# Performance work log

Measured on AMD Instinct MI355X. Metric: run time of the kernel, lower is better.

The kernel has to match this reference:

```python
import jax, jax.numpy as jnp
import numpy as np

B, S, CTX, DIM = 2, 2048, 2048, 2048
H, HKV, HD = 16, 4, 128
HID = 5464  # 4*ceil(int(4*DIM*2/3)/4)
EPS = 1.1920929e-07  # torch eps=None -> finfo(fp32).eps
REP = H // HKV


def rmsnorm(x, w):
    return x * jax.lax.rsqrt(jnp.mean(x * x, axis=-1, keepdims=True) + EPS) * w


def rotate_half(x):
    # interleaved rotate: out[::2] = -x[1::2], out[1::2] = x[::2]
    x2 = x.reshape(x.shape[:-1] + (-1, 2))
    return jnp.stack([-x2[..., 1], x2[..., 0]], axis=-1).reshape(x.shape)


def masked_attn(q, k, v, mask):
    # q,k,v: [B,H,Sq/Sk,D]; mask broadcastable to [B,H,Sq,Sk]
    scale = 1.0 / jnp.sqrt(jnp.asarray(q.shape[-1], q.dtype))
    s = jnp.einsum('bhqd,bhkd->bhqk', q, k) * scale
    s = jnp.where(mask, s, jnp.asarray(-1e30, s.dtype))
    p = jax.nn.softmax(s, axis=-1)
    p = jnp.where(mask, p, 0.0)  # fully-masked rows -> 0 output (flex_attention semantics)
    return jnp.einsum('bhqk,bhkd->bhqd', p, v)


def setup_inputs() -> dict:
    key = jax.random.key(0)
    ks = jax.random.split(key, 20)
    std = 0.02
    return {
        'x': jax.random.normal(ks[0], (B, S, DIM), jnp.float32),
        'context': jax.random.normal(ks[1], (B, CTX, DIM), jnp.float32),
        'freqs_cos': jax.random.uniform(ks[2], (S, 1, HD), jnp.float32),
        'freqs_sin': jax.random.uniform(ks[3], (S, 1, HD), jnp.float32),
        'wqkv': jax.random.normal(ks[4], ((H + 2 * HKV) * HD, DIM), jnp.float32) * std,
        'wo_self': jax.random.normal(ks[5], (DIM, DIM), jnp.float32) * std,
        'qn_self': jnp.ones((HD,), jnp.float32),
        'kn_self': jnp.ones((HD,), jnp.float32),
        'wq': jax.random.normal(ks[6], (H * HD, DIM), jnp.float32) * std,
        'wkv': jax.random.normal(ks[7], (2 * HKV * HD, DIM), jnp.float32) * std,
        'wo_cross': jax.random.normal(ks[8], (DIM, DIM), jnp.float32) * std,
        'qn_cross': jnp.ones((HD,), jnp.float32),
        'kn_cross': jnp.ones((HD,), jnp.float32),
        'w1': jax.random.normal(ks[9], (HID, DIM), jnp.float32) * std,
        'w2': jax.random.normal(ks[10], (DIM, HID), jnp.float32) * std,
        'attn_norm_w': jnp.ones((DIM,), jnp.float32),
        'cross_norm_w': jnp.ones((DIM,), jnp.float32),
        'ffn_norm_w': jnp.ones((DIM,), jnp.float32),
        'vis_mask': jax.random.randint(ks[11], (B, S), 0, 2).astype(bool),
        'context_mask': jax.random.randint(ks[12], (B, CTX), 0, 2).astype(bool),
    }


def reference(x, context, freqs_cos, freqs_sin, wqkv, wo_self, qn_self, kn_self,
              wq, wkv, wo_cross, qn_cross, kn_cross, w1, w2,
              attn_norm_w, cross_norm_w, ffn_norm_w, vis_mask, context_mask):
    b, s, _ = x.shape
    ctx = context.shape[1]

    # ---- self-attention (prenorm) ----
    h0 = rmsnorm(x, attn_norm_w)
    qkv = h0 @ wqkv.T
    xq = qkv[..., :H * HD].reshape(b, s, H, HD)
    xk = qkv[..., H * HD:(H + HKV) * HD].reshape(b, s, HKV, HD)
    xv = qkv[..., (H + HKV) * HD:].reshape(b, s, HKV, HD)
    xq = rmsnorm(xq, qn_self)   # qk-norm BEFORE rope in self-attn
    xk = rmsnorm(xk, kn_self)
    xq = xq * freqs_cos + rotate_half(xq) * freqs_sin
    xk = xk * freqs_cos + rotate_half(xk) * freqs_sin
    q = xq.transpose(0, 2, 1, 3)
    k = jnp.repeat(xk.transpose(0, 2, 1, 3), REP, axis=1)
    v = jnp.repeat(xv.transpose(0, 2, 1, 3), REP, axis=1)
    m_self = vis_mask[:, None, :, None] & vis_mask[:, None, None, :]
    a = masked_attn(q, k, v, m_self)
    h = x + a.transpose(0, 2, 1, 3).reshape(b, s, DIM) @ wo_self.T

    # ---- cross-attention (prenorm) ----
    hc = rmsnorm(h, cross_norm_w)
    xq = (hc @ wq.T).reshape(b, s, H, HD)
    kv = context @ wkv.T
    xk = kv[..., :HKV * HD].reshape(b, ctx, HKV, HD)
    xv = kv[..., HKV * HD:].reshape(b, ctx, HKV, HD)
    xq = xq * freqs_cos + rotate_half(xq) * freqs_sin  # rope on q BEFORE qk-norm in cross-attn
    xq = rmsnorm(xq, qn_cross)
    xk = rmsnorm(xk, kn_cross)
    q = xq.transpose(0, 2, 1, 3)
    k = jnp.repeat(xk.transpose(0, 2, 1, 3), REP, axis=1)
    v = jnp.repeat(xv.transpose(0, 2, 1, 3), REP, axis=1)
    m_cross = context_mask[:, None, None, :]
    a = masked_attn(q, k, v, m_cross)
    h = h + a.transpose(0, 2, 1, 3).reshape(b, s, DIM) @ wo_cross.T

    # ---- FFN (silu) ----
    hf = rmsnorm(h, ffn_norm_w)
    return h + jax.nn.silu(hf @ w1.T) @ w2.T
```

## Files before the change

### kernel.cpp

```cpp
#include <hip/hip_runtime.h>

#define DEVI __device__ __forceinline__

typedef __attribute__((ext_vector_type(4))) float f32x4;
typedef __attribute__((ext_vector_type(8))) __bf16 bf16x8;

static constexpr float EPS = 1.1920929e-07f;
static constexpr float SC2L = 0.12751551960234575f;

DEVI float bf2f(unsigned short u){ return __uint_as_float(((unsigned)u)<<16); }
DEVI unsigned short f2bfu(float f){
  unsigned u = __float_as_uint(f);
  u += 0x7fffu + ((u>>16)&1u);
  return (unsigned short)(u>>16);
}
DEVI unsigned pack2(float a, float b){ return (unsigned)f2bfu(a) | ((unsigned)f2bfu(b)<<16); }
DEVI float exp2a(float x){ float r; asm("v_exp_f32 %0, %1" : "=v"(r) : "v"(x)); return r; }
DEVI unsigned cvtpk(float lo, float hi){
  unsigned r; asm("v_cvt_pk_bf16_f32 %0, %1, %2" : "=v"(r) : "v"(lo), "v"(hi)); return r;
}

DEVI void gload16(const void* g, const void* l){
  __builtin_amdgcn_global_load_lds((const __attribute__((address_space(1))) void*)g,
                                   (__attribute__((address_space(3))) void*)l, 16, 0, 0);
}

__global__ void k_masknorm(const unsigned* __restrict__ vin, const unsigned* __restrict__ cin,
                           unsigned char* __restrict__ vout, unsigned char* __restrict__ cout){
  __shared__ int smode;
  const int t = threadIdx.x;
  if (t==0) smode = 0;
  __syncthreads();
  unsigned loc = 0;
  for (int i=t; i<1024; i+=256) loc |= (vin[i] > 1u);
  if (loc) smode = 1;
  __syncthreads();
  if (smode){
    for (int i=t; i<1024; i+=256){
      ((unsigned*)vout)[i] = vin[i];
      ((unsigned*)cout)[i] = cin[i];
    }
  } else {
    const int* vi = (const int*)vin; const int* ci = (const int*)cin;
    for (int i=t; i<4096; i+=256){
      vout[i] = (unsigned char)(vi[i] != 0);
      cout[i] = (unsigned char)(ci[i] != 0);
    }
  }
}

__global__ void k_conv(const float* __restrict__ s, unsigned short* __restrict__ d, int n4){
  int i = blockIdx.x*256 + threadIdx.x;
  if (i >= n4) return;
  float4 v = ((const float4*)s)[i];
  uint2 u; u.x = pack2(v.x, v.y); u.y = pack2(v.z, v.w);
  ((uint2*)d)[i] = u;
}
__global__ void k_convpad_rows(const float* __restrict__ s, unsigned short* __restrict__ d,
                               int R, int C, int Rp){
  int i = blockIdx.x*256 + threadIdx.x;
  int total = (Rp*C)>>2;
  if (i >= total) return;
  uint2 u; u.x = 0u; u.y = 0u;
  if (i*4 < R*C){ float4 v = ((const float4*)s)[i]; u.x = pack2(v.x,v.y); u.y = pack2(v.z,v.w); }
  ((uint2*)d)[i] = u;
}
__global__ void k_convpad_cols(const float* __restrict__ s, unsigned short* __restrict__ d,
                               int N, int K, int Kp){
  int i = blockIdx.x*256 + threadIdx.x;
  int total = (N*Kp)>>2;
  if (i >= total) return;
  int i4 = i*4; int n = i4/Kp; int k = i4 - n*Kp;
  uint2 u; u.x = 0u; u.y = 0u;
  if (k < K){ float4 v = *(const float4*)(s + (size_t)n*K + k); u.x = pack2(v.x,v.y); u.y = pack2(v.z,v.w); }
  ((uint2*)d)[i] = u;
}

__global__ void k_rms(const float* __restrict__ X, const float* __restrict__ W,
                      unsigned short* __restrict__ Y){
  const int row = blockIdx.x, tid = threadIdx.x;
  const float* x = X + (size_t)row*2048;
  float4 v0 = ((const float4*)x)[tid*2];
  float4 v1 = ((const float4*)x)[tid*2+1];
  float ss = v0.x*v0.x+v0.y*v0.y+v0.z*v0.z+v0.w*v0.w
           + v1.x*v1.x+v1.y*v1.y+v1.z*v1.z+v1.w*v1.w;
  #pragma unroll
  for (int o=32;o;o>>=1) ss += __shfl_xor(ss, o);
  __shared__ float red[4];
  if ((tid&63)==0) red[tid>>6] = ss;
  __syncthreads();
  float tot = red[0]+red[1]+red[2]+red[3];
  float rs = rsqrtf(tot*(1.0f/2048.0f) + EPS);
  float4 w0 = ((const float4*)W)[tid*2];
  float4 w1 = ((const float4*)W)[tid*2+1];
  uint4 u;
  u.x = pack2(v0.x*rs*w0.x, v0.y*rs*w0.y);
  u.y = pack2(v0.z*rs*w0.z, v0.w*rs*w0.w);
  u.z = pack2(v1.x*rs*w1.x, v1.y*rs*w1.y);
  u.w = pack2(v1.z*rs*w1.z, v1.w*rs*w1.w);
  *(uint4*)(Y + (size_t)row*2048 + tid*8) = u;
}

template<int EPI>
__global__ void k_gemm(const unsigned short* __restrict__ A, const unsigned short* __restrict__ Bw,
                       void* Cout, const float* resid, int M, int N, int K){
  __shared__ __align__(16) unsigned short sm[16384];
  const int tid = threadIdx.x;
  const int w = tid>>6, l = tid&63, g = l>>4, q = l&15;
  const int bm = blockIdx.y<<7, bn = blockIdx.x<<7;
  const int wr = (w>>1)<<6, wc = (w&1)<<6;
  f32x4 acc[4][4];
  #pragma unroll
  for (int a=0;a<4;++a)
    #pragma unroll
    for (int b2=0;b2<4;++b2) acc[a][b2] = f32x4{0.f,0.f,0.f,0.f};

  const unsigned short* Ag = A + (size_t)bm*K;
  const unsigned short* Bg = Bw + (size_t)bn*K;
  const int nk = K>>5;
  int cur = 0;

  auto STAGE = [&](int buf, int kt){
    #pragma unroll
    for (int i=0;i<2;++i){
      int L = (i*256+tid)*16;
      int r = L>>6; int ce = (L&63)>>1;
      int lofs = __builtin_amdgcn_readfirstlane(buf*8192 + i*4096 + (tid>>6)*1024);
      gload16(Ag + (size_t)r*K + (kt<<5) + ce, (const char*)sm + lofs);
    }
    #pragma unroll
    for (int i=0;i<2;++i){
      int L = (i*256+tid)*16;
      int r = L>>6; int ce = (L&63)>>1;
      int lofs = __builtin_amdgcn_readfirstlane(16384 + buf*8192 + i*4096 + (tid>>6)*1024);
      gload16(Bg + (size_t)r*K + (kt<<5) + ce, (const char*)sm + lofs);
    }
  };

  STAGE(0, 0);
  __syncthreads();
  for (int kt=0; kt<nk; ++kt){
    if (kt+1 < nk) STAGE(cur^1, kt+1);
    const unsigned short* Ab = sm + cur*4096;
    const unsigned short* Bb = sm + 8192 + cur*4096;
    bf16x8 af[4], bfr[4];
    #pragma unroll
    for (int mi=0;mi<4;++mi) af[mi] = *(const bf16x8*)(Ab + (wr + mi*16 + q)*32 + g*8);
    #pragma unroll
    for (int ni=0;ni<4;++ni) bfr[ni] = *(const bf16x8*)(Bb + (wc + ni*16 + q)*32 + g*8);
    #pragma unroll
    for (int mi=0;mi<4;++mi)
      #pragma unroll
      for (int ni=0;ni<4;++ni)
        acc[mi][ni] = __builtin_amdgcn_mfma_f32_16x16x32_bf16(af[mi], bfr[ni], acc[mi][ni], 0,0,0);
    __syncthreads();
    cur ^= 1;
  }
  #pragma unroll
  for (int mi=0;mi<4;++mi)
    #pragma unroll
    for (int ni=0;ni<4;++ni)
      #pragma unroll
      for (int r=0;r<4;++r){
        int row = bm + wr + mi*16 + g*4 + r;
        int col = bn + wc + ni*16 + q;
        size_t idx = (size_t)row*N + col;
        float v = acc[mi][ni][r];
        if (EPI==0) ((unsigned short*)Cout)[idx] = f2bfu(v);
        else if (EPI==1){ float sg = v/(1.0f+__expf(-v)); ((unsigned short*)Cout)[idx] = f2bfu(sg); }
        else ((float*)Cout)[idx] = resid[idx] + v;
      }
}

__global__ void k_self_pp(const unsigned short* __restrict__ qkv, const float* __restrict__ fc,
                          const float* __restrict__ fs, const float* __restrict__ qn,
                          const float* __restrict__ kn,
                          unsigned short* __restrict__ Qb, unsigned short* __restrict__ Kb,
                          unsigned short* __restrict__ Vt){
  const int row = blockIdx.x;
  const int b = row>>11, s = row&2047;
  const int w = threadIdx.x>>6, l = threadIdx.x&63;
  const int d0 = 2*l, d1 = d0+1;
  const float c0 = fc[s*128+d0], c1 = fc[s*128+d1];
  const float s0 = fs[s*128+d0], s1 = fs[s*128+d1];
  #pragma unroll
  for (int it=0; it<6; ++it){
    const int hh = it*4 + w;
    const unsigned short* src = qkv + (size_t)row*3072 + hh*128;
    if (hh >= 20){
      const int hv = hh - 20;
      size_t base = ((size_t)(b*4 + hv))*128*2048;
      Vt[base + (size_t)d0*2048 + s] = src[d0];
      Vt[base + (size_t)d1*2048 + s] = src[d1];
    } else {
      float x0 = bf2f(src[d0]), x1 = bf2f(src[d1]);
      float ss = x0*x0 + x1*x1;
      #pragma unroll
      for (int o=32;o;o>>=1) ss += __shfl_xor(ss, o);
      float rs = rsqrtf(ss*(1.0f/128.0f) + EPS);
      if (hh < 16){
        float y0 = x0*rs*qn[d0], y1 = x1*rs*qn[d1];
        *(unsigned*)(Qb + (((size_t)(b*16 + hh)*2048 + s)*128) + d0)
          = pack2((y0*c0 - y1*s0)*SC2L, (y1*c1 + y0*s1)*SC2L);
      } else {
        float y0 = x0*rs*kn[d0], y1 = x1*rs*kn[d1];
        *(unsigned*)(Kb + (((size_t)(b*4 + (hh-16))*2048 + s)*128) + d0)
          = pack2(y0*c0 - y1*s0, y1*c1 + y0*s1);
      }
    }
  }
}

__global__ void k_crossq_pp(const unsigned short* __restrict__ qc, const float* __restrict__ fc,
                            const float* __restrict__ fs, const float* __restrict__ qn,
                            unsigned short* __restrict__ Qb){
  const int row = blockIdx.x;
  const int b = row>>11, s = row&2047;
  const int w = threadIdx.x>>6, l = threadIdx.x&63;
  const int d0 = 2*l, d1 = d0+1;
  const float c0 = fc[s*128+d0], c1 = fc[s*128+d1];
  const float s0 = fs[s*128+d0], s1 = fs[s*128+d1];
  #pragma unroll
  for (int it=0; it<4; ++it){
    const int hh = it*4 + w;
    const unsigned short* src = qc + (size_t)row*2048 + hh*128;
    float x0 = bf2f(src[d0]), x1 = bf2f(src[d1]);
    float y0 = x0*c0 - x1*s0;
    float y1 = x1*c1 + x0*s1;
    float ss = y0*y0 + y1*y1;
    #pragma unroll
    for (int o=32;o;o>>=1) ss += __shfl_xor(ss, o);
    float rs = rsqrtf(ss*(1.0f/128.0f) + EPS);
    *(unsigned*)(Qb + (((size_t)(b*16 + hh)*2048 + s)*128) + d0)
      = pack2(y0*rs*qn[d0]*SC2L, y1*rs*qn[d1]*SC2L);
  }
}

__global__ void k_crosskv_pp(const unsigned short* __restrict__ kvc, const float* __restrict__ kn,
                             unsigned short* __restrict__ Kb, unsigned short* __restrict__ Vt){
  const int row = blockIdx.x;
  const int b = row>>11, s = row&2047;
  const int w = threadIdx.x>>6, l = threadIdx.x&63;
  const int d0 = 2*l, d1 = d0+1;
  #pragma unroll
  for (int it=0; it<2; ++it){
    const int hh = it*4 + w;
    const unsigned short* src = kvc + (size_t)row*1024 + hh*128;
    if (hh < 4){
      float x0 = bf2f(src[d0]), x1 = bf2f(src[d1]);
      float ss = x0*x0 + x1*x1;
      #pragma unroll
      for (int o=32;o;o>>=1) ss += __shfl_xor(ss, o);
      float rs = rsqrtf(ss*(1.0f/128.0f) + EPS);
      *(unsigned*)(Kb + (((size_t)(b*4 + hh)*2048 + s)*128) + d0)
        = pack2(x0*rs*kn[d0], x1*rs*kn[d1]);
    } else {
      const int hv = hh-4;
      size_t base = ((size_t)(b*4 + hv))*128*2048;
      Vt[base + (size_t)d0*2048 + s] = src[d0];
      Vt[base + (size_t)d1*2048 + s] = src[d1];
    }
  }
}

template<bool QMASK>
__global__ void k_attn(const unsigned short* __restrict__ Qg, const unsigned short* __restrict__ Kg,
                       const unsigned short* __restrict__ Vtg,
                       const unsigned char* __restrict__ qm, const unsigned char* __restrict__ km,
                       unsigned short* __restrict__ Og, int H, int HKV){
  constexpr int SK = 2048, SQ = 2048, NT = SK/64;
  __shared__ __align__(16) char smem[81920];
  const int qt = blockIdx.x, h = blockIdx.y, b = blockIdx.z;
  const int hk = h / (H/HKV);
  const int tid = threadIdx.x, w = tid>>6, l = tid&63, g = l>>4, q = l&15;

  {
    const unsigned long long mv = ((const unsigned long long*)(km + (size_t)b*SK))[tid];
    float* bl = (float*)(smem + 73728);
    #pragma unroll
    for (int j=0;j<8;++j)
      bl[tid*8+j] = ((mv>>(8*j)) & 0xffull) ? 0.0f : -3.0e38f;
  }

  const size_t qrow = (size_t)(b*H + h)*SQ + qt*64 + w*16 + q;
  bf16x8 qf[4];
  #pragma unroll
  for (int ks=0;ks<4;++ks) qf[ks] = *(const bf16x8*)(Qg + qrow*128 + ks*32 + g*8);

  f32x4 oacc[8];
  #pragma unroll
  for (int i=0;i<8;++i) oacc[i] = f32x4{0.f,0.f,0.f,0.f};
  float m_run = -1.0e30f, l_run = 0.f;

  const unsigned short* Kt0 = Kg + (size_t)(b*HKV + hk)*SK*128;
  const unsigned short* Vt0 = Vtg + (size_t)(b*HKV + hk)*128*SK;
  const float* biasf = (const float*)(smem + 73728);
  char* Pl = smem + 65536 + w*2048;

  auto STAGE_T = [&](int t, int p){
    #pragma unroll
    for (int i=0;i<4;++i){
      int L = (i*256+tid)*16;
      int r = L>>8, c16 = (L>>4)&15;
      int c = (c16 & 8) | ((c16 & 7) ^ (r & 7));
      int lofs = __builtin_amdgcn_readfirstlane(p*16384 + i*4096 + w*1024);
      gload16(Kt0 + (size_t)(t*64 + r)*128 + c*8, smem + lofs);
    }
    #pragma unroll
    for (int i=0;i<4;++i){
      int L = (i*256+tid)*16;
      int d = L>>7, c8 = (L>>4)&7;
      int c = c8 ^ (d & 7);
      int lofs = __builtin_amdgcn_readfirstlane(32768 + p*16384 + i*4096 + w*1024);
      gload16(Vt0 + (size_t)d*SK + t*64 + c*8, smem + lofs);
    }
  };

  STAGE_T(0, 0);

  for (int t=0; t<NT; ++t){
    const int p = t&1;
    asm volatile("s_waitcnt lgkmcnt(0)" ::: "memory");
    __builtin_amdgcn_s_barrier();
    asm volatile("" ::: "memory");
    if (t+1 < NT){
      STAGE_T(t+1, p^1);
      asm volatile("s_waitcnt vmcnt(8)" ::: "memory");
    } else {
      asm volatile("s_waitcnt vmcnt(0)" ::: "memory");
    }
    __builtin_amdgcn_s_barrier();
    asm volatile("" ::: "memory");

    const char* Kb_ = smem + p*16384;
    const char* Vb_ = smem + 32768 + p*16384;

    f32x4 sacc[4];
    #pragma unroll
    for (int i=0;i<4;++i) sacc[i] = f32x4{0.f,0.f,0.f,0.f};
    __builtin_amdgcn_s_setprio(1);
    #pragma unroll
    for (int ks=0;ks<4;++ks){
      #pragma unroll
      for (int mi=0;mi<4;++mi){
        int kcol = mi*16 + q;
        int c = 4*ks + g;
        int c16 = (c & 8) | ((c & 7) ^ (kcol & 7));
        bf16x8 ak = *(const bf16x8*)(Kb_ + kcol*256 + c16*16);
        sacc[mi] = __builtin_amdgcn_mfma_f32_16x16x32_bf16(ak, qf[ks], sacc[mi], 0,0,0);
      }
    }
    __builtin_amdgcn_s_setprio(0);

    float sv[4][4];
    float mloc = -3.0e38f;
    #pragma unroll
    for (int mi=0;mi<4;++mi){
      f32x4 bb = *(const f32x4*)(biasf + t*64 + mi*16 + g*4);
      #pragma unroll
      for (int r=0;r<4;++r){
        float v = sacc[mi][r] + bb[r];
        sv[mi][r] = v;
        mloc = fmaxf(mloc, v);
      }
    }
    mloc = fmaxf(mloc, __shfl_xor(mloc, 16));
    mloc = fmaxf(mloc, __shfl_xor(mloc, 32));
    if (!__all(mloc - m_run <= 8.0f)){
      float mnew = fmaxf(m_run, mloc);
      float alpha = exp2a(m_run - mnew);
      l_run *= alpha;
      #pragma unroll
      for (int i=0;i<8;++i) oacc[i] *= alpha;
      m_run = mnew;
    }
    float rsum = 0.f;
    unsigned pb[4][2];
    #pragma unroll
    for (int mi=0;mi<4;++mi){
      float p0 = exp2a(sv[mi][0] - m_run);
      float p1 = exp2a(sv[mi][1] - m_run);
      float p2 = exp2a(sv[mi][2] - m_run);
      float p3 = exp2a(sv[mi][3] - m_run);
      rsum += (p0+p1)+(p2+p3);
      pb[mi][0] = cvtpk(p0, p1);
      pb[mi][1] = cvtpk(p2, p3);
    }
    rsum += __shfl_xor(rsum, 16);
    rsum += __shfl_xor(rsum, 32);
    l_run += rsum;

    #pragma unroll
    for (int mi=0;mi<4;++mi){
      int c16 = (2*mi + (g>>1)) ^ (q & 7);
      uint2 uu; uu.x = pb[mi][0]; uu.y = pb[mi][1];
      *(uint2*)(Pl + q*128 + c16*16 + (g&1)*8) = uu;
    }
    asm volatile("" ::: "memory");

    __builtin_amdgcn_s_setprio(1);
    #pragma unroll
    for (int ks=0;ks<2;++ks){
      int c16 = (4*ks + g) ^ (q & 7);
      bf16x8 pf = *(const bf16x8*)(Pl + q*128 + c16*16);
      #pragma unroll
      for (int mi=0;mi<8;++mi){
        int d = mi*16 + q;
        bf16x8 vf = *(const bf16x8*)(Vb_ + d*128 + c16*16);
        oacc[mi] = __builtin_amdgcn_mfma_f32_16x16x32_bf16(vf, pf, oacc[mi], 0,0,0);
      }
    }
    __builtin_amdgcn_s_setprio(0);
  }

  float inv = (l_run > 0.f) ? 1.0f/l_run : 0.f;
  if (QMASK){
    if (!qm[(size_t)b*SQ + qt*64 + w*16 + q]) inv = 0.f;
  }
  __syncthreads();
  float* Ot = (float*)smem;
  #pragma unroll
  for (int mi=0;mi<8;++mi)
    #pragma unroll
    for (int r=0;r<4;++r){
      int d = mi*16 + g*4 + r;
      Ot[d*65 + w*16 + q] = oacc[mi][r]*inv;
    }
  __syncthreads();
  int qloc = tid>>2, seg = tid&3;
  int srow = qt*64 + qloc;
  size_t obase = ((size_t)b*SQ + srow)*(size_t)(H*128) + (size_t)h*128 + seg*32;
  #pragma unroll
  for (int p4=0;p4<4;++p4){
    float vv[8];
    #pragma unroll
    for (int j=0;j<8;++j) vv[j] = Ot[(seg*32 + p4*8 + j)*65 + qloc];
    uint4 u;
    u.x = pack2(vv[0],vv[1]); u.y = pack2(vv[2],vv[3]);
    u.z = pack2(vv[4],vv[5]); u.w = pack2(vv[6],vv[7]);
    *(uint4*)(Og + obase + p4*8) = u;
  }
}

extern "C" void kernel_launch(void* const* d_in, const int* in_sizes, int n_in,
                              void* d_out, int out_size, void* d_ws, size_t ws_size,
                              hipStream_t stream){
  const float* x        = (const float*)d_in[0];
  const float* ctx      = (const float*)d_in[1];
  const float* fc       = (const float*)d_in[2];
  const float* fs       = (const float*)d_in[3];
  const float* wqkv     = (const float*)d_in[4];
  const float* wo_self  = (const float*)d_in[5];
  const float* qn_self  = (const float*)d_in[6];
  const float* kn_self  = (const float*)d_in[7];
  const float* wq       = (const float*)d_in[8];
  const float* wkv      = (const float*)d_in[9];
  const float* wo_cross = (const float*)d_in[10];
  const float* qn_cross = (const float*)d_in[11];
  const float* kn_cross = (const float*)d_in[12];
  const float* w1       = (const float*)d_in[13];
  const float* w2       = (const float*)d_in[14];
  const float* attn_nw  = (const float*)d_in[15];
  const float* cross_nw = (const float*)d_in[16];
  const float* ffn_nw   = (const float*)d_in[17];
  const unsigned* vis_raw   = (const unsigned*)d_in[18];
  const unsigned* cmask_raw = (const unsigned*)d_in[19];
  float* out = (float*)d_out;

  char* ws = (char*)d_ws;
  unsigned short* wslot = (unsigned short*)(ws);
  unsigned short* ctxbf = (unsigned short*)(ws +  22544384);
  unsigned short* nbuf  = (unsigned short*)(ws +  39321600);
  unsigned short* qkvb  = (unsigned short*)(ws +  56098816);
  unsigned short* Qb    = (unsigned short*)(ws +  81264640);
  unsigned short* Kb    = (unsigned short*)(ws +  98041856);
  unsigned short* Vtb   = (unsigned short*)(ws + 102236160);
  unsigned short* aob   = (unsigned short*)(ws + 106430464);
  unsigned short* midb  = (unsigned short*)(ws + 123207680);
  unsigned char*  visN  = (unsigned char*)(ws + 168296448);
  unsigned char*  cmkN  = (unsigned char*)(ws + 168300544);
  unsigned short* qcb   = qkvb;
  unsigned short* kvcb  = qkvb + 8388608;

  auto conv = [&](const float* s, unsigned short* dst, size_t n){
    int n4 = (int)(n>>2);
    k_conv<<<(n4+255)/256, 256, 0, stream>>>(s, dst, n4);
  };

  k_masknorm<<<1,256,0,stream>>>(vis_raw, cmask_raw, visN, cmkN);

  conv(ctx, ctxbf, (size_t)4096*2048);
  k_rms<<<4096,256,0,stream>>>(x, attn_nw, nbuf);
  conv(wqkv, wslot, (size_t)3072*2048);
  k_gemm<0><<<dim3(24,32),256,0,stream>>>(nbuf, wslot, qkvb, nullptr, 4096,3072,2048);
  k_self_pp<<<4096,256,0,stream>>>(qkvb, fc, fs, qn_self, kn_self, Qb, Kb, Vtb);
  k_attn<true><<<dim3(32,16,2),256,0,stream>>>(Qb, Kb, Vtb, visN, visN, aob, 16, 4);
  conv(wo_self, wslot, (size_t)2048*2048);
  k_gemm<2><<<dim3(16,32),256,0,stream>>>(aob, wslot, out, x, 4096,2048,2048);

  k_rms<<<4096,256,0,stream>>>(out, cross_nw, nbuf);
  conv(wq, wslot, (size_t)2048*2048);
  k_gemm<0><<<dim3(16,32),256,0,stream>>>(nbuf, wslot, qcb, nullptr, 4096,2048,2048);
  conv(wkv, wslot, (size_t)1024*2048);
  k_gemm<0><<<dim3(8,32),256,0,stream>>>(ctxbf, wslot, kvcb, nullptr, 4096,1024,2048);
  k_crossq_pp<<<4096,256,0,stream>>>(qcb, fc, fs, qn_cross, Qb);
  k_crosskv_pp<<<4096,256,0,stream>>>(kvcb, kn_cross, Kb, Vtb);
  k_attn<false><<<dim3(32,16,2),256,0,stream>>>(Qb, Kb, Vtb, nullptr, cmkN, aob, 16, 4);
  conv(wo_cross, wslot, (size_t)2048*2048);
  k_gemm<2><<<dim3(16,32),256,0,stream>>>(aob, wslot, out, out, 4096,2048,2048);

  k_rms<<<4096,256,0,stream>>>(out, ffn_nw, nbuf);
  k_convpad_rows<<<(5504*2048/4+255)/256,256,0,stream>>>(w1, wslot, 5464, 2048, 5504);
  k_gemm<1><<<dim3(43,32),256,0,stream>>>(nbuf, wslot, midb, nullptr, 4096,5504,2048);
  k_convpad_cols<<<(2048*5504/4+255)/256,256,0,stream>>>(w2, wslot, 2048, 5464, 5504);
  k_gemm<2><<<dim3(16,32),256,0,stream>>>(midb, wslot, out, out, 4096,2048,5504);

  (void)in_sizes; (void)n_in; (void)out_size; (void)ws_size;
}
```

Measured before the change: 906.4 us.

## Add triple-buffered 128x256 GEMM with swizzled LDS and use it for large projections

Adds a new GEMM kernel with 512 threads, 128x256 output tiles, K-step 64, a three-stage LDS ring filled by direct global-to-LDS loads, an XOR swizzle to avoid bank conflicts, and raised wave priority around the MFMA block. Most projection GEMMs switch to it, and the FFN hidden size is padded to 5632 to fit the 256-wide tiles. The goal is better overlap of memory loads with matrix math and more reuse per tile. In exchange it uses one block per CU with a large LDS footprint, does extra work on the padded columns, and now shares one workspace buffer between midb and aob.

New measurement: 826.9 us. -8.8%, faster.

```diff
diff --git a/kernel.cpp b/kernel.cpp
--- a/kernel.cpp
+++ b/kernel.cpp
@@ -164,6 +164,103 @@
       for (int r=0;r<4;++r){
         int row = bm + wr + mi*16 + g*4 + r;
         int col = bn + wc + ni*16 + q;
+        size_t idx = (size_t)row*N + col;
+        float v = acc[mi][ni][r];
+        if (EPI==0) ((unsigned short*)Cout)[idx] = f2bfu(v);
+        else if (EPI==1){ float sg = v/(1.0f+__expf(-v)); ((unsigned short*)Cout)[idx] = f2bfu(sg); }
+        else ((float*)Cout)[idx] = resid[idx] + v;
+      }
+}
+
+template<int EPI>
+__global__ __launch_bounds__(512,1)
+void k_gemm2(const unsigned short* __restrict__ A, const unsigned short* __restrict__ Bw,
+             void* Cout, const float* resid, int M, int N, int K){
+  __shared__ __align__(16) char sm[147456];
+  const int tid = threadIdx.x;
+  const int wid = tid>>6, l = tid&63, g = l>>4, q = l&15;
+  const int wm = wid>>2, wn = wid&3;
+  const int bm = blockIdx.y<<7, bn = blockIdx.x<<8;
+  f32x4 acc[4][4];
+  #pragma unroll
+  for (int a=0;a<4;++a)
+    #pragma unroll
+    for (int b2=0;b2<4;++b2) acc[a][b2] = f32x4{0.f,0.f,0.f,0.f};
+
+  const unsigned short* Ag = A + (size_t)bm*K;
+  const unsigned short* Bg = Bw + (size_t)bn*K;
+  const int nk = K>>6;
+
+  auto STAGE_A = [&](int buf, int kt){
+    #pragma unroll
+    for (int j=0;j<2;++j){
+      int L = (j*512+tid)*16;
+      int lr = L>>7, c8 = (L>>4)&7;
+      int cg = c8 ^ (lr&7);
+      int lofs = __builtin_amdgcn_readfirstlane(buf*49152 + j*8192 + wid*1024);
+      gload16(Ag + (size_t)lr*K + (kt<<6) + cg*8, sm + lofs);
+    }
+  };
+  auto STAGE_B1 = [&](int buf, int kt, int j){
+    int L = (j*512+tid)*16;
+    int rn = L>>7, c8 = (L>>4)&7;
+    int cg = c8 ^ (rn&7);
+    int lofs = __builtin_amdgcn_readfirstlane(buf*49152 + 16384 + j*8192 + wid*1024);
+    gload16(Bg + (size_t)rn*K + (kt<<6) + cg*8, sm + lofs);
+  };
+
+  STAGE_A(0,0); STAGE_B1(0,0,0); STAGE_B1(0,0,1); STAGE_B1(0,0,2); STAGE_B1(0,0,3);
+  STAGE_A(1,1); STAGE_B1(1,1,0); STAGE_B1(1,1,1); STAGE_B1(1,1,2); STAGE_B1(1,1,3);
+
+  int buf = 0;
+  for (int kt=0; kt<nk; ++kt){
+    int p2 = buf+2; if (p2>2) p2-=3;
+    if (kt+1 < nk) asm volatile("s_waitcnt vmcnt(6)" ::: "memory");
+    else           asm volatile("s_waitcnt vmcnt(0)" ::: "memory");
+    asm volatile("s_waitcnt lgkmcnt(0)" ::: "memory");
+    __builtin_amdgcn_s_barrier();
+    asm volatile("" ::: "memory");
+
+    const char* Ab = sm + buf*49152;
+    const char* Bb = sm + buf*49152 + 16384;
+
+    #pragma unroll
+    for (int ks=0; ks<2; ++ks){
+      if (kt+2 < nk){
+        if (ks==0){ STAGE_A(p2, kt+2); STAGE_B1(p2, kt+2, 0); }
+        else      { STAGE_B1(p2, kt+2, 1); STAGE_B1(p2, kt+2, 2); STAGE_B1(p2, kt+2, 3); }
+      }
+      bf16x8 af[4], bfr[4];
+      #pragma unroll
+      for (int mi=0;mi<4;++mi){
+        int lr = wm*64 + mi*16 + q;
+        af[mi] = *(const bf16x8*)(Ab + lr*128 + (((ks*4+g) ^ (lr&7))<<4));
+      }
+      #pragma unroll
+      for (int ni=0;ni<4;++ni){
+        int rn = wn*64 + ni*16 + q;
+        bfr[ni] = *(const bf16x8*)(Bb + rn*128 + (((ks*4+g) ^ (rn&7))<<4));
+      }
+      asm volatile("s_waitcnt lgkmcnt(0)" ::: "memory");
+      __builtin_amdgcn_s_setprio(1);
+      #pragma unroll
+      for (int mi=0;mi<4;++mi)
+        #pragma unroll
+        for (int ni=0;ni<4;++ni)
+          acc[mi][ni] = __builtin_amdgcn_mfma_f32_16x16x32_bf16(af[mi], bfr[ni], acc[mi][ni], 0,0,0);
+      __builtin_amdgcn_s_setprio(0);
+    }
+    buf = (buf==2) ? 0 : buf+1;
+  }
+
+  #pragma unroll
+  for (int mi=0;mi<4;++mi)
+    #pragma unroll
+    for (int ni=0;ni<4;++ni)
+      #pragma unroll
+      for (int r=0;r<4;++r){
+        int row = bm + wm*64 + mi*16 + g*4 + r;
+        int col = bn + wn*64 + ni*16 + q;
         size_t idx = (size_t)row*N + col;
         float v = acc[mi][ni][r];
         if (EPI==0) ((unsigned short*)Cout)[idx] = f2bfu(v);
@@ -469,16 +566,16 @@
 
   char* ws = (char*)d_ws;
   unsigned short* wslot = (unsigned short*)(ws);
-  unsigned short* ctxbf = (unsigned short*)(ws +  22544384);
-  unsigned short* nbuf  = (unsigned short*)(ws +  39321600);
-  unsigned short* qkvb  = (unsigned short*)(ws +  56098816);
-  unsigned short* Qb    = (unsigned short*)(ws +  81264640);
-  unsigned short* Kb    = (unsigned short*)(ws +  98041856);
-  unsigned short* Vtb   = (unsigned short*)(ws + 102236160);
-  unsigned short* aob   = (unsigned short*)(ws + 106430464);
-  unsigned short* midb  = (unsigned short*)(ws + 123207680);
-  unsigned char*  visN  = (unsigned char*)(ws + 168296448);
-  unsigned char*  cmkN  = (unsigned char*)(ws + 168300544);
+  unsigned short* ctxbf = (unsigned short*)(ws +  23068672);
+  unsigned short* nbuf  = (unsigned short*)(ws +  39845888);
+  unsigned short* qkvb  = (unsigned short*)(ws +  56623104);
+  unsigned short* Qb    = (unsigned short*)(ws +  81788928);
+  unsigned short* Kb    = (unsigned short*)(ws +  98566144);
+  unsigned short* Vtb   = (unsigned short*)(ws + 102760448);
+  unsigned short* aob   = (unsigned short*)(ws + 106954752);
+  unsigned short* midb  = (unsigned short*)(ws + 106954752);
+  unsigned char*  visN  = (unsigned char*)(ws + 153092096);
+  unsigned char*  cmkN  = (unsigned char*)(ws + 153096192);
   unsigned short* qcb   = qkvb;
   unsigned short* kvcb  = qkvb + 8388608;
 
@@ -492,28 +589,28 @@
   conv(ctx, ctxbf, (size_t)4096*2048);
   k_rms<<<4096,256,0,stream>>>(x, attn_nw, nbuf);
   conv(wqkv, wslot, (size_t)3072*2048);
-  k_gemm<0><<<dim3(24,32),256,0,stream>>>(nbuf, wslot, qkvb, nullptr, 4096,3072,2048);
+  k_gemm2<0><<<dim3(12,32),512,0,stream>>>(nbuf, wslot, qkvb, nullptr, 4096,3072,2048);
   k_self_pp<<<4096,256,0,stream>>>(qkvb, fc, fs, qn_self, kn_self, Qb, Kb, Vtb);
   k_attn<true><<<dim3(32,16,2),256,0,stream>>>(Qb, Kb, Vtb, visN, visN, aob, 16, 4);
   conv(wo_self, wslot, (size_t)2048*2048);
-  k_gemm<2><<<dim3(16,32),256,0,stream>>>(aob, wslot, out, x, 4096,2048,2048);
+  k_gemm2<2><<<dim3(8,32),512,0,stream>>>(aob, wslot, out, x, 4096,2048,2048);
 
   k_rms<<<4096,256,0,stream>>>(out, cross_nw, nbuf);
   conv(wq, wslot, (size_t)2048*2048);
-  k_gemm<0><<<dim3(16,32),256,0,stream>>>(nbuf, wslot, qcb, nullptr, 4096,2048,2048);
+  k_gemm2<0><<<dim3(8,32),512,0,stream>>>(nbuf, wslot, qcb, nullptr, 4096,2048,2048);
   conv(wkv, wslot, (size_t)1024*2048);
   k_gemm<0><<<dim3(8,32),256,0,stream>>>(ctxbf, wslot, kvcb, nullptr, 4096,1024,2048);
   k_crossq_pp<<<4096,256,0,stream>>>(qcb, fc, fs, qn_cross, Qb);
   k_crosskv_pp<<<4096,256,0,stream>>>(kvcb, kn_cross, Kb, Vtb);
   k_attn<false><<<dim3(32,16,2),256,0,stream>>>(Qb, Kb, Vtb, nullptr, cmkN, aob, 16, 4);
   conv(wo_cross, wslot, (size_t)2048*2048);
-  k_gemm<2><<<dim3(16,32),256,0,stream>>>(aob, wslot, out, out, 4096,2048,2048);
+  k_gemm2<2><<<dim3(8,32),512,0,stream>>>(aob, wslot, out, out, 4096,2048,2048);
 
   k_rms<<<4096,256,0,stream>>>(out, ffn_nw, nbuf);
-  k_convpad_rows<<<(5504*2048/4+255)/256,256,0,stream>>>(w1, wslot, 5464, 2048, 5504);
-  k_gemm<1><<<dim3(43,32),256,0,stream>>>(nbuf, wslot, midb, nullptr, 4096,5504,2048);
-  k_convpad_cols<<<(2048*5504/4+255)/256,256,0,stream>>>(w2, wslot, 2048, 5464, 5504);
-  k_gemm<2><<<dim3(16,32),256,0,stream>>>(midb, wslot, out, out, 4096,2048,5504);
+  k_convpad_rows<<<(5632*2048/4+255)/256,256,0,stream>>>(w1, wslot, 5464, 2048, 5632);
+  k_gemm2<1><<<dim3(22,32),512,0,stream>>>(nbuf, wslot, midb, nullptr, 4096,5632,2048);
+  k_convpad_cols<<<(2048*5632/4+255)/256,256,0,stream>>>(w2, wslot, 2048, 5464, 5632);
+  k_gemm2<2><<<dim3(8,32),512,0,stream>>>(midb, wslot, out, out, 4096,2048,5632);
 
   (void)in_sizes; (void)n_in; (void)out_size; (void)ws_size;
 }
```
